# Optimization experiments

Hardware: AMD Instinct MI355X
Metric: run time of the kernel (lower is better)

Reference implementation:

```python
import jax, jax.numpy as jnp
import numpy as np

B, S, D = 4, 4096, 1024
EPS_LN = 1e-5
EPS_REC = 1e-8


def _layernorm(x, g, b):
    mu = jnp.mean(x, axis=-1, keepdims=True)
    var = jnp.mean((x - mu) ** 2, axis=-1, keepdims=True)
    return (x - mu) * jax.lax.rsqrt(var + EPS_LN) * g + b


def setup_inputs() -> dict:
    key = jax.random.key(0)
    ks = jax.random.split(key, 8)
    scale = 1.0 / np.sqrt(D)
    return {
        "x": jax.random.normal(ks[0], (B, S, D), dtype=jnp.float32),
        "x_prev": jax.random.normal(ks[1], (B, S, D), dtype=jnp.float32),
        "mu": jnp.float32(0.5),
        "decay_w": jax.random.uniform(ks[2], (D, 1), jnp.float32, -scale, scale),
        "decay_b": jnp.zeros((1,), jnp.float32),
        "ln1_g": jnp.ones((D,), jnp.float32),
        "ln1_b": jnp.zeros((D,), jnp.float32),
        "Wr_w": jax.random.uniform(ks[3], (D, D), jnp.float32, -scale, scale),
        "Wr_b": jnp.zeros((D,), jnp.float32),
        "Wv_w": jax.random.uniform(ks[4], (D, D), jnp.float32, -scale, scale),
        "Wv_b": jnp.zeros((D,), jnp.float32),
        "ln2_g": jnp.ones((D,), jnp.float32),
        "ln2_b": jnp.zeros((D,), jnp.float32),
    }


def reference(x, x_prev, mu, decay_w, decay_b, ln1_g, ln1_b,
              Wr_w, Wr_b, Wv_w, Wv_b, ln2_g, ln2_b):
    # Shift (token-mix by scalar mu)
    shifted = mu * x + (1.0 - mu) * x_prev  # [B,S,D]

    # SequenceMergingSeq with C = V = W = shifted
    decay = jax.nn.sigmoid(jnp.einsum("bsd,do->bso", shifted, decay_w) + decay_b)  # [B,S,1]
    e = jnp.exp(shifted)                       # [B,S,D]
    ea = jnp.sum(e, axis=-1, keepdims=True)    # [B,S,1]
    ev = e * shifted                           # [B,S,D]

    def step(carry, inp):
        a, b = carry
        d_t, ea_t, ev_t = inp
        a = d_t * a + ea_t            # [B,1]
        b = d_t * b + ev_t            # [B,D]
        return (a, b), b / (a + EPS_REC)

    init = (jnp.zeros((B, 1), shifted.dtype), jnp.zeros((B, D), shifted.dtype))
    xs = (jnp.swapaxes(decay, 0, 1), jnp.swapaxes(ea, 0, 1), jnp.swapaxes(ev, 0, 1))
    _, out_sbd = jax.lax.scan(step, init, xs)  # [S,B,D]
    merged = _layernorm(jnp.swapaxes(out_sbd, 0, 1), ln1_g, ln1_b)  # [B,S,D]

    # StateCoupling
    gate = jax.nn.sigmoid(jnp.einsum("bsd,ed->bse", merged, Wr_w) + Wr_b)
    value = jnp.einsum("bsd,ed->bse", merged, Wv_w) + Wv_b
    coupled = _layernorm(gate * value, ln2_g, ln2_b)

    return shifted + coupled
```

## Files before the change

kernel.cpp:

```cpp
#include <hip/hip_runtime.h>

#define BATCH 4
#define SEQ   4096
#define DIM   1024
#define NCH   512
#define CHK   8
#define NROWS (BATCH*SEQ)
#define NKT   32

typedef __attribute__((ext_vector_type(4))) float f32x4;
typedef __attribute__((ext_vector_type(8))) short shortx8;
typedef __attribute__((ext_vector_type(4))) short shortx4;

static __device__ __forceinline__ unsigned short f2bf(float f){
    unsigned int u = __float_as_uint(f);
    u += 0x7FFFu + ((u >> 16) & 1u);
    return (unsigned short)(u >> 16);
}
static __device__ __forceinline__ float bf2f(unsigned short h){
    return __uint_as_float(((unsigned int)h) << 16);
}
static __device__ __forceinline__ float sigmoidf_fast(float x){
    return 1.0f / (1.0f + __expf(-x));
}
static __device__ __forceinline__ shortx4 pack4(f32x4 s){
    shortx4 o;
    o.x = (short)f2bf(s.x); o.y = (short)f2bf(s.y);
    o.z = (short)f2bf(s.z); o.w = (short)f2bf(s.w);
    return o;
}
static __device__ __forceinline__ f32x4 unpack4(shortx4 s){
    f32x4 o;
    o.x = bf2f((unsigned short)s.x); o.y = bf2f((unsigned short)s.y);
    o.z = bf2f((unsigned short)s.z); o.w = bf2f((unsigned short)s.w);
    return o;
}

__global__ __launch_bounds__(256) void k_shift_scan(
    const float* __restrict__ X, const float* __restrict__ XP,
    const float* __restrict__ mu_p, const float* __restrict__ dw,
    const float* __restrict__ db_p,
    const float* __restrict__ Wr, const float* __restrict__ Wv,
    unsigned short* __restrict__ Wcat,
    unsigned short* __restrict__ shifted,
    unsigned short* __restrict__ b_local, float* __restrict__ a_local,
    float* __restrict__ cumP)
{
    const int tid  = threadIdx.x;

    if (blockIdx.x >= 512){
        const int pb = blockIdx.x - 512;
        #pragma unroll 4
        for (int i = 0; i < 32; ++i){
            const int n = pb*32 + i;
            const int grp = n >> 5, r = n & 31;
            const float* src = (r < 16) ? (Wr + (size_t)(grp*16 + r)*DIM)
                                        : (Wv + (size_t)(grp*16 + (r-16))*DIM);
            f32x4 v = reinterpret_cast<const f32x4*>(src)[tid];
            reinterpret_cast<shortx4*>(Wcat)[n*256 + tid] = pack4(v);
        }
        return;
    }

    const int lane = tid & 63;
    const int wid  = tid >> 6;
    const int cid  = blockIdx.x*4 + wid;
    const int batch = cid >> 9;
    const int chunk = cid & (NCH-1);
    const int row0  = batch*SEQ + chunk*CHK;

    const float mu = mu_p[0];
    const float om = 1.0f - mu;
    const float db = db_p[0];

    const f32x4* dwv = reinterpret_cast<const f32x4*>(dw);
    const f32x4 w0 = dwv[lane], w1 = dwv[64+lane], w2 = dwv[128+lane], w3 = dwv[192+lane];

    f32x4 b0 = {0,0,0,0}, b1 = {0,0,0,0}, b2 = {0,0,0,0}, b3 = {0,0,0,0};
    float a_run = 0.f, cp = 1.f;

    const f32x4* Xv  = reinterpret_cast<const f32x4*>(X);
    const f32x4* XPv = reinterpret_cast<const f32x4*>(XP);
    shortx4* BL = reinterpret_cast<shortx4*>(b_local);
    shortx4* SH = reinterpret_cast<shortx4*>(shifted);

    for (int r = 0; r < CHK; ++r){
        const int row = row0 + r;
        const int rb  = row*(DIM/4);

        f32x4 x0 = Xv[rb+lane],     x1 = Xv[rb+64+lane],
              x2 = Xv[rb+128+lane], x3 = Xv[rb+192+lane];
        f32x4 p0 = XPv[rb+lane],     p1 = XPv[rb+64+lane],
              p2 = XPv[rb+128+lane], p3 = XPv[rb+192+lane];
        f32x4 s0 = mu*x0 + om*p0, s1 = mu*x1 + om*p1;
        f32x4 s2 = mu*x2 + om*p2, s3 = mu*x3 + om*p3;

        SH[rb+lane]     = pack4(s0);
        SH[rb+64+lane]  = pack4(s1);
        SH[rb+128+lane] = pack4(s2);
        SH[rb+192+lane] = pack4(s3);

        float dot = s0.x*w0.x + s0.y*w0.y + s0.z*w0.z + s0.w*w0.w
                  + s1.x*w1.x + s1.y*w1.y + s1.z*w1.z + s1.w*w1.w
                  + s2.x*w2.x + s2.y*w2.y + s2.z*w2.z + s2.w*w2.w
                  + s3.x*w3.x + s3.y*w3.y + s3.z*w3.z + s3.w*w3.w;

        f32x4 e0, e1, e2, e3;
        e0.x=__expf(s0.x); e0.y=__expf(s0.y); e0.z=__expf(s0.z); e0.w=__expf(s0.w);
        e1.x=__expf(s1.x); e1.y=__expf(s1.y); e1.z=__expf(s1.z); e1.w=__expf(s1.w);
        e2.x=__expf(s2.x); e2.y=__expf(s2.y); e2.z=__expf(s2.z); e2.w=__expf(s2.w);
        e3.x=__expf(s3.x); e3.y=__expf(s3.y); e3.z=__expf(s3.z); e3.w=__expf(s3.w);
        float ea = e0.x+e0.y+e0.z+e0.w + e1.x+e1.y+e1.z+e1.w
                 + e2.x+e2.y+e2.z+e2.w + e3.x+e3.y+e3.z+e3.w;

        #pragma unroll
        for (int off = 1; off < 64; off <<= 1){
            dot += __shfl_xor(dot, off, 64);
            ea  += __shfl_xor(ea,  off, 64);
        }

        const float dt = sigmoidf_fast(dot + db);
        a_run = dt*a_run + ea;
        cp   *= dt;
        b0 = dt*b0 + e0*s0;  b1 = dt*b1 + e1*s1;
        b2 = dt*b2 + e2*s2;  b3 = dt*b3 + e3*s3;

        BL[rb+lane]     = pack4(b0);
        BL[rb+64+lane]  = pack4(b1);
        BL[rb+128+lane] = pack4(b2);
        BL[rb+192+lane] = pack4(b3);
        if (lane == 0){ a_local[row] = a_run; cumP[row] = cp; }
    }
}

__global__ __launch_bounds__(64) void k_combine(
    const unsigned short* __restrict__ b_local, const float* __restrict__ a_local,
    const float* __restrict__ cumP,
    float* __restrict__ carryA, unsigned short* __restrict__ carryB)
{
    const int batch = blockIdx.x >> 2;
    const int dseg  = blockIdx.x & 3;
    const int tid = threadIdx.x;
    const int d0 = dseg*256 + tid*4;

    __shared__ float sP[NCH], sA[NCH];
    for (int c = tid; c < NCH; c += 64){
        const int er = batch*SEQ + c*CHK + (CHK-1);
        sP[c] = cumP[er];
        sA[c] = a_local[er];
    }
    __syncthreads();

    const unsigned short* bl = b_local + (size_t)batch*SEQ*DIM + d0;
    unsigned short* cB = carryB + (size_t)batch*NCH*DIM + d0;
    const bool wA = (dseg == 0 && tid == 0);
    float* cAp = carryA + batch*NCH;

    shortx4 pf[16];
    #pragma unroll
    for (int i = 0; i < 16; ++i)
        pf[i] = *reinterpret_cast<const shortx4*>(bl + (i*CHK + CHK-1)*DIM);

    f32x4 cb = {0,0,0,0};
    float ca = 0.f;

    for (int cc = 0; cc < NCH; cc += 16){
        const bool more = (cc + 16 < NCH);
        #pragma unroll
        for (int k = 0; k < 16; ++k){
            const int c = cc + k;
            f32x4 v = unpack4(pf[k]);
            if (more)
                pf[k] = *reinterpret_cast<const shortx4*>(bl + ((c+16)*CHK + CHK-1)*DIM);
            *reinterpret_cast<shortx4*>(cB + (size_t)c*DIM) = pack4(cb);
            if (wA) cAp[c] = ca;
            const float p = sP[c];
            cb = p*cb + v;
            ca = p*ca + sA[c];
        }
    }
}

__global__ __launch_bounds__(256) void k_fix_ln1(
    const unsigned short* __restrict__ b_local, const float* __restrict__ a_local,
    const float* __restrict__ cumP, const float* __restrict__ carryA,
    const unsigned short* __restrict__ carryB,
    const float* __restrict__ g1, const float* __restrict__ bb1,
    unsigned short* __restrict__ merged)
{
    const int tid = threadIdx.x, lane = tid & 63, wid = tid >> 6;
    const int row = blockIdx.x*4 + wid;
    const int batch = row >> 12;
    const int c = (row & (SEQ-1)) >> 3;

    const float cpv = cumP[row];
    const float a = a_local[row] + cpv * carryA[batch*NCH + c];
    const float inv_a = 1.0f / (a + 1e-8f);

    const shortx4* BL = reinterpret_cast<const shortx4*>(b_local) + (size_t)row*256;
    const shortx4* CB = reinterpret_cast<const shortx4*>(carryB) + (size_t)(batch*NCH + c)*256;

    f32x4 o[4];
    float s = 0.f, s2 = 0.f;
    #pragma unroll
    for (int j = 0; j < 4; ++j){
        f32x4 bl = unpack4(BL[j*64 + lane]);
        f32x4 cb = unpack4(CB[j*64 + lane]);
        f32x4 v = (bl + cpv*cb) * inv_a;
        o[j] = v;
        s  += v.x+v.y+v.z+v.w;
        s2 += v.x*v.x + v.y*v.y + v.z*v.z + v.w*v.w;
    }
    #pragma unroll
    for (int off = 1; off < 64; off <<= 1){
        s  += __shfl_xor(s,  off, 64);
        s2 += __shfl_xor(s2, off, 64);
    }
    const float mean = s * (1.0f/DIM);
    const float rstd = rsqrtf(s2*(1.0f/DIM) - mean*mean + 1e-5f);
    shortx4* MG = reinterpret_cast<shortx4*>(merged) + (size_t)row*256;
    #pragma unroll
    for (int j = 0; j < 4; ++j){
        f32x4 gg = reinterpret_cast<const f32x4*>(g1)[j*64 + lane];
        f32x4 bb = reinterpret_cast<const f32x4*>(bb1)[j*64 + lane];
        MG[j*64 + lane] = pack4((o[j] - mean)*rstd*gg + bb);
    }
}

typedef __attribute__((address_space(3))) unsigned int lds_uint;
typedef __attribute__((address_space(1))) unsigned int glob_uint;
static __device__ __forceinline__ void gload16(const unsigned short* g, char* l){
    __builtin_amdgcn_global_load_lds((const glob_uint*)g, (lds_uint*)l, 16, 0, 0);
}
#define SBAR() do { __builtin_amdgcn_sched_barrier(0); __builtin_amdgcn_s_barrier(); __builtin_amdgcn_sched_barrier(0); } while(0)
#define LGKM0() do { asm volatile("s_waitcnt lgkmcnt(0)" ::: "memory"); __builtin_amdgcn_sched_barrier(0); } while(0)
#define VMC(n)  asm volatile("s_waitcnt vmcnt(" #n ")" ::: "memory")
#define LDSE 136

__global__ __launch_bounds__(512, 2) void k_gemm(
    const unsigned short* __restrict__ A,
    const unsigned short* __restrict__ Bt,
    const float* __restrict__ rbias, const float* __restrict__ vbias,
    unsigned short* __restrict__ gv)
{
    __shared__ __align__(16) char lds[69632];
    const int tid  = threadIdx.x;
    const int lane = tid & 63;
    const int wid  = tid >> 6;
    const int wm   = wid >> 2;
    const int wn   = wid & 3;

    const int bid  = blockIdx.x;
    const int wgid = (bid & 7)*64 + (bid >> 3);
    const int mt = wgid >> 3, nt = wgid & 7;
    const int m0 = mt*256, n0 = nt*256;

    const int rin = lane >> 2;
    const int scg = (lane & 3) ^ (((lane >> 5) & 1) << 1);
    const unsigned short* gA = A  + (size_t)(m0 + wid*32 + rin)*DIM + scg*8;
    const unsigned short* gB = Bt + (size_t)(n0 + wid*32 + rin)*DIM + scg*8;

    const int fr = lane & 15, fq = lane >> 4;
    const int soff = fr*64 + ((fq*16) ^ ((fr & 8) ? 32 : 0));

    f32x4 acc[8][4];
    #pragma unroll
    for (int i = 0; i < 8; ++i)
        #pragma unroll
        for (int j = 0; j < 4; ++j) acc[i][j] = (f32x4){0,0,0,0};

    auto STAGE = [&](int tk){
        char* da = lds + (tk & 1)*32768 + wid*2048;
        const unsigned short* sa = gA + tk*32;
        gload16(sa,          da);
        gload16(sa + 16*DIM, da + 1024);
        char* db = lds + (tk & 1)*32768 + 16384 + wid*2048;
        const unsigned short* sb = gB + tk*32;
        gload16(sb,          db);
        gload16(sb + 16*DIM, db + 1024);
    };

    shortx8 afA[8], bfA[4], afB[8], bfB[4];

    #define LOADF(AF, BF, bb) do {                                              \
        _Pragma("unroll")                                                       \
        for (int mf = 0; mf < 8; ++mf)                                          \
            AF[mf] = *reinterpret_cast<const shortx8*>((bb) + (wm*8 + mf)*1024 + soff); \
        _Pragma("unroll")                                                       \
        for (int nf = 0; nf < 4; ++nf)                                          \
            BF[nf] = *reinterpret_cast<const shortx8*>((bb) + 16384 + (wn*4 + nf)*1024 + soff); \
    } while (0)

    #define MFMA32(AF, BF) do {                                                 \
        __builtin_amdgcn_s_setprio(1);                                          \
        _Pragma("unroll")                                                       \
        for (int mf = 0; mf < 8; ++mf)                                          \
            _Pragma("unroll")                                                   \
            for (int nf = 0; nf < 4; ++nf)                                      \
                acc[mf][nf] = __builtin_amdgcn_mfma_f32_16x16x32_bf16(          \
                    AF[mf], BF[nf], acc[mf][nf], 0, 0, 0);                      \
        __builtin_amdgcn_s_setprio(0);                                          \
    } while (0)

    #define BODY(T, AFc, BFc, AFn, BFn) do {                                    \
        LGKM0();                                                                \
        SBAR();                          \
        if ((T) + 2 < NKT){ STAGE((T) + 2); VMC(4); }                           \
        else if ((T) + 2 == NKT){ VMC(0); }                                     \
        SBAR();                          \
        if ((T) + 1 < NKT){ LOADF(AFn, BFn, lds + (((T) + 1) & 1)*32768); }     \
        __builtin_amdgcn_sched_barrier(0);                                      \
        MFMA32(AFc, BFc);                                                       \
    } while (0)

    STAGE(0); STAGE(1);
    VMC(4);
    SBAR();
    LOADF(afA, bfA, lds);

    for (int T = 0; T < NKT; T += 2){
        BODY(T,     afA, bfA, afB, bfB);
        BODY(T + 1, afB, bfB, afA, bfA);
    }

    __syncthreads();
    unsigned short* ep = reinterpret_cast<unsigned short*>(lds);
    #pragma unroll
    for (int pr = 0; pr < 2; ++pr){
        const int el = wn*32 + pr*16 + fr;
        const float rbe = rbias[nt*128 + el];
        const float vbe = vbias[nt*128 + el];
        #pragma unroll
        for (int mf = 0; mf < 8; ++mf){
            const int rbase = wm*128 + mf*16 + fq*4;
            f32x4 ga = acc[mf][2*pr], va = acc[mf][2*pr+1];
            #pragma unroll
            for (int q = 0; q < 4; ++q){
                const float g = sigmoidf_fast(ga[q] + rbe);
                ep[(rbase + q)*LDSE + el] = f2bf(g*(va[q] + vbe));
            }
        }
    }
    __syncthreads();
    #pragma unroll
    for (int p = 0; p < 8; ++p){
        const int r  = p*32 + (tid >> 4);
        const int c8 = tid & 15;
        shortx8 val = *reinterpret_cast<const shortx8*>(&ep[r*LDSE + c8*8]);
        *reinterpret_cast<shortx8*>(&gv[(size_t)(m0 + r)*DIM + nt*128 + c8*8]) = val;
    }
    #undef BODY
    #undef MFMA32
    #undef LOADF
}

__global__ __launch_bounds__(256) void k_ln2_res(
    const unsigned short* __restrict__ gvb, const unsigned short* __restrict__ shifted,
    const float* __restrict__ g2, const float* __restrict__ b2,
    float* __restrict__ out)
{
    const int tid = threadIdx.x, lane = tid & 63, wid = tid >> 6;
    const int row = blockIdx.x*4 + wid;

    const shortx4* GV = reinterpret_cast<const shortx4*>(gvb) + (size_t)row*256;
    const shortx4* SH = reinterpret_cast<const shortx4*>(shifted) + (size_t)row*256;

    f32x4 v[4];
    float s = 0.f, s2 = 0.f;
    #pragma unroll
    for (int j = 0; j < 4; ++j){
        f32x4 x = unpack4(GV[j*64 + lane]);
        v[j] = x;
        s  += x.x+x.y+x.z+x.w;
        s2 += x.x*x.x + x.y*x.y + x.z*x.z + x.w*x.w;
    }
    #pragma unroll
    for (int off = 1; off < 64; off <<= 1){
        s  += __shfl_xor(s,  off, 64);
        s2 += __shfl_xor(s2, off, 64);
    }
    const float mean = s * (1.0f/DIM);
    const float rstd = rsqrtf(s2*(1.0f/DIM) - mean*mean + 1e-5f);
    f32x4* O = reinterpret_cast<f32x4*>(out) + (size_t)row*256;
    #pragma unroll
    for (int j = 0; j < 4; ++j){
        f32x4 gg = reinterpret_cast<const f32x4*>(g2)[j*64 + lane];
        f32x4 bb = reinterpret_cast<const f32x4*>(b2)[j*64 + lane];
        f32x4 sh = unpack4(SH[j*64 + lane]);
        O[j*64 + lane] = sh + (v[j] - mean)*rstd*gg + bb;
    }
}

extern "C" void kernel_launch(void* const* d_in, const int* in_sizes, int n_in,
                              void* d_out, int out_size, void* d_ws, size_t ws_size,
                              hipStream_t stream)
{
    (void)in_sizes; (void)n_in; (void)out_size; (void)ws_size;
    const float* x     = (const float*)d_in[0];
    const float* xprev = (const float*)d_in[1];
    const float* mu    = (const float*)d_in[2];
    const float* dw    = (const float*)d_in[3];
    const float* db    = (const float*)d_in[4];
    const float* ln1g  = (const float*)d_in[5];
    const float* ln1b  = (const float*)d_in[6];
    const float* Wr    = (const float*)d_in[7];
    const float* Wrb   = (const float*)d_in[8];
    const float* Wv    = (const float*)d_in[9];
    const float* Wvb   = (const float*)d_in[10];
    const float* ln2g  = (const float*)d_in[11];
    const float* ln2b  = (const float*)d_in[12];
    float* out = (float*)d_out;

    char* ws = (char*)d_ws;
    size_t off = 0;
    auto alloc = [&](size_t bytes) -> void* {
        void* p = ws + off;
        off += (bytes + 255) & ~(size_t)255;
        return p;
    };
    unsigned short* shifted = (unsigned short*)alloc((size_t)NROWS*DIM*2);
    unsigned short* b_local = (unsigned short*)alloc((size_t)NROWS*DIM*2);
    unsigned short* merged  = (unsigned short*)alloc((size_t)NROWS*DIM*2);
    unsigned short* carryB  = (unsigned short*)alloc((size_t)BATCH*NCH*DIM*2);
    unsigned short* Wcat    = (unsigned short*)alloc((size_t)2048*1024*2);
    float* a_local          = (float*)alloc((size_t)NROWS*4);
    float* cumP             = (float*)alloc((size_t)NROWS*4);
    float* carryA           = (float*)alloc((size_t)BATCH*NCH*4);
    unsigned short* gvbuf   = b_local;

    hipLaunchKernelGGL(k_shift_scan, dim3(576),  dim3(256), 0, stream,
                       x, xprev, mu, dw, db, Wr, Wv, Wcat, shifted, b_local, a_local, cumP);
    hipLaunchKernelGGL(k_combine,    dim3(16),   dim3(64),  0, stream,
                       b_local, a_local, cumP, carryA, carryB);
    hipLaunchKernelGGL(k_fix_ln1,    dim3(4096), dim3(256), 0, stream,
                       b_local, a_local, cumP, carryA, carryB, ln1g, ln1b, merged);
    hipLaunchKernelGGL(k_gemm,       dim3(512),  dim3(512), 0, stream,
                       merged, Wcat, Wrb, Wvb, gvbuf);
    hipLaunchKernelGGL(k_ln2_res,    dim3(4096), dim3(256), 0, stream,
                       gvbuf, shifted, ln2g, ln2b, out);
}
```

Baseline: 210.6 us.

## Restructure GEMM to 4 waves with 128x128 per-wave tiles and simpler pipeline

The fused gate/value GEMM now runs with 256 threads (4 waves) per block instead of 512. Each wave computes an 8x8 grid of MFMA fragments rather than 8x4, and the software-pipelined fragment double-buffering is replaced by a single-buffered load-then-compute loop with a global prefetch two tiles ahead. The epilogue is split into two halves so the LDS staging buffer still fits. This raises arithmetic intensity per wave and cuts LDS fragment reads, but it roughly doubles accumulator registers, halves waves per CU, and loses overlap of LDS reads with MFMA.

```diff
diff --git a/kernel.cpp b/kernel.cpp
--- a/kernel.cpp
+++ b/kernel.cpp
@@ -234,10 +234,10 @@
 }
 #define SBAR() do { __builtin_amdgcn_sched_barrier(0); __builtin_amdgcn_s_barrier(); __builtin_amdgcn_sched_barrier(0); } while(0)
 #define LGKM0() do { asm volatile("s_waitcnt lgkmcnt(0)" ::: "memory"); __builtin_amdgcn_sched_barrier(0); } while(0)
-#define VMC(n)  asm volatile("s_waitcnt vmcnt(" #n ")" ::: "memory")
+#define VMC(n)  do { asm volatile("s_waitcnt vmcnt(" #n ")" ::: "memory"); __builtin_amdgcn_sched_barrier(0); } while(0)
 #define LDSE 136
 
-__global__ __launch_bounds__(512, 2) void k_gemm(
+__global__ __launch_bounds__(256, 1) void k_gemm(
     const unsigned short* __restrict__ A,
     const unsigned short* __restrict__ Bt,
     const float* __restrict__ rbias, const float* __restrict__ vbias,
@@ -247,8 +247,8 @@
     const int tid  = threadIdx.x;
     const int lane = tid & 63;
     const int wid  = tid >> 6;
-    const int wm   = wid >> 2;
-    const int wn   = wid & 3;
+    const int wm   = wid >> 1;
+    const int wn   = wid & 1;
 
     const int bid  = blockIdx.x;
     const int wgid = (bid & 7)*64 + (bid >> 3);
@@ -257,101 +257,95 @@
 
     const int rin = lane >> 2;
     const int scg = (lane & 3) ^ (((lane >> 5) & 1) << 1);
-    const unsigned short* gA = A  + (size_t)(m0 + wid*32 + rin)*DIM + scg*8;
-    const unsigned short* gB = Bt + (size_t)(n0 + wid*32 + rin)*DIM + scg*8;
+    const unsigned short* gA = A  + (size_t)(m0 + wid*64 + rin)*DIM + scg*8;
+    const unsigned short* gB = Bt + (size_t)(n0 + wid*64 + rin)*DIM + scg*8;
 
     const int fr = lane & 15, fq = lane >> 4;
     const int soff = fr*64 + ((fq*16) ^ ((fr & 8) ? 32 : 0));
 
-    f32x4 acc[8][4];
+    f32x4 acc[8][8];
     #pragma unroll
     for (int i = 0; i < 8; ++i)
         #pragma unroll
-        for (int j = 0; j < 4; ++j) acc[i][j] = (f32x4){0,0,0,0};
+        for (int j = 0; j < 8; ++j) acc[i][j] = (f32x4){0,0,0,0};
 
     auto STAGE = [&](int tk){
-        char* da = lds + (tk & 1)*32768 + wid*2048;
+        char* base = lds + (tk & 1)*32768;
         const unsigned short* sa = gA + tk*32;
-        gload16(sa,          da);
-        gload16(sa + 16*DIM, da + 1024);
-        char* db = lds + (tk & 1)*32768 + 16384 + wid*2048;
         const unsigned short* sb = gB + tk*32;
-        gload16(sb,          db);
-        gload16(sb + 16*DIM, db + 1024);
+        #pragma unroll
+        for (int s = 0; s < 4; ++s){
+            gload16(sa + (size_t)(s*16)*DIM, base + (wid*4 + s)*1024);
+            gload16(sb + (size_t)(s*16)*DIM, base + 16384 + (wid*4 + s)*1024);
+        }
     };
 
-    shortx8 afA[8], bfA[4], afB[8], bfB[4];
-
-    #define LOADF(AF, BF, bb) do {                                              \
-        _Pragma("unroll")                                                       \
-        for (int mf = 0; mf < 8; ++mf)                                          \
-            AF[mf] = *reinterpret_cast<const shortx8*>((bb) + (wm*8 + mf)*1024 + soff); \
-        _Pragma("unroll")                                                       \
-        for (int nf = 0; nf < 4; ++nf)                                          \
-            BF[nf] = *reinterpret_cast<const shortx8*>((bb) + 16384 + (wn*4 + nf)*1024 + soff); \
-    } while (0)
-
-    #define MFMA32(AF, BF) do {                                                 \
-        __builtin_amdgcn_s_setprio(1);                                          \
-        _Pragma("unroll")                                                       \
-        for (int mf = 0; mf < 8; ++mf)                                          \
-            _Pragma("unroll")                                                   \
-            for (int nf = 0; nf < 4; ++nf)                                      \
-                acc[mf][nf] = __builtin_amdgcn_mfma_f32_16x16x32_bf16(          \
-                    AF[mf], BF[nf], acc[mf][nf], 0, 0, 0);                      \
-        __builtin_amdgcn_s_setprio(0);                                          \
-    } while (0)
-
-    #define BODY(T, AFc, BFc, AFn, BFn) do {                                    \
-        LGKM0();                                                                \
-        SBAR();                          \
-        if ((T) + 2 < NKT){ STAGE((T) + 2); VMC(4); }                           \
-        else if ((T) + 2 == NKT){ VMC(0); }                                     \
-        SBAR();                          \
-        if ((T) + 1 < NKT){ LOADF(AFn, BFn, lds + (((T) + 1) & 1)*32768); }     \
-        __builtin_amdgcn_sched_barrier(0);                                      \
-        MFMA32(AFc, BFc);                                                       \
-    } while (0)
+    shortx8 af[8], bf[8];
 
     STAGE(0); STAGE(1);
-    VMC(4);
+    VMC(8);
     SBAR();
-    LOADF(afA, bfA, lds);
-
-    for (int T = 0; T < NKT; T += 2){
-        BODY(T,     afA, bfA, afB, bfB);
-        BODY(T + 1, afB, bfB, afA, bfA);
-    }
-
-    __syncthreads();
-    unsigned short* ep = reinterpret_cast<unsigned short*>(lds);
-    #pragma unroll
-    for (int pr = 0; pr < 2; ++pr){
-        const int el = wn*32 + pr*16 + fr;
-        const float rbe = rbias[nt*128 + el];
-        const float vbe = vbias[nt*128 + el];
-        #pragma unroll
-        for (int mf = 0; mf < 8; ++mf){
-            const int rbase = wm*128 + mf*16 + fq*4;
-            f32x4 ga = acc[mf][2*pr], va = acc[mf][2*pr+1];
+
+    for (int T = 0; T < NKT; ++T){
+        const char* base = lds + (T & 1)*32768;
+
+        #pragma unroll
+        for (int m = 0; m < 8; ++m)
+            af[m] = *reinterpret_cast<const shortx8*>(base + (wm*8 + m)*1024 + soff);
+        #pragma unroll
+        for (int n = 0; n < 8; ++n)
+            bf[n] = *reinterpret_cast<const shortx8*>(base + 16384 + (wn*8 + n)*1024 + soff);
+        LGKM0();
+        SBAR();
+
+        if (T + 2 < NKT) STAGE(T + 2);
+
+        __builtin_amdgcn_s_setprio(1);
+        #pragma unroll
+        for (int m = 0; m < 8; ++m)
             #pragma unroll
-            for (int q = 0; q < 4; ++q){
-                const float g = sigmoidf_fast(ga[q] + rbe);
-                ep[(rbase + q)*LDSE + el] = f2bf(g*(va[q] + vbe));
+            for (int n = 0; n < 8; ++n)
+                acc[m][n] = __builtin_amdgcn_mfma_f32_16x16x32_bf16(af[m], bf[n], acc[m][n], 0, 0, 0);
+        __builtin_amdgcn_s_setprio(0);
+
+        if (T + 1 < NKT){
+            if (T + 2 < NKT) { VMC(8); } else { VMC(0); }
+            SBAR();
+        }
+    }
+
+    #pragma unroll
+    for (int half = 0; half < 2; ++half){
+        __syncthreads();
+        unsigned short* ep = reinterpret_cast<unsigned short*>(lds);
+        if (wm == half){
+            #pragma unroll
+            for (int j = 0; j < 4; ++j){
+                const int ecol = wn*64 + j*16 + fr;
+                const float rbe = rbias[nt*128 + ecol];
+                const float vbe = vbias[nt*128 + ecol];
+                #pragma unroll
+                for (int m = 0; m < 8; ++m){
+                    const int rbase = m*16 + fq*4;
+                    f32x4 ga = acc[m][2*j], va = acc[m][2*j+1];
+                    #pragma unroll
+                    for (int q = 0; q < 4; ++q){
+                        const float g = sigmoidf_fast(ga[q] + rbe);
+                        ep[(rbase + q)*LDSE + ecol] = f2bf(g*(va[q] + vbe));
+                    }
+                }
             }
         }
-    }
-    __syncthreads();
-    #pragma unroll
-    for (int p = 0; p < 8; ++p){
-        const int r  = p*32 + (tid >> 4);
-        const int c8 = tid & 15;
-        shortx8 val = *reinterpret_cast<const shortx8*>(&ep[r*LDSE + c8*8]);
-        *reinterpret_cast<shortx8*>(&gv[(size_t)(m0 + r)*DIM + nt*128 + c8*8]) = val;
-    }
-    #undef BODY
-    #undef MFMA32
-    #undef LOADF
+        __syncthreads();
+        #pragma unroll
+        for (int p = 0; p < 8; ++p){
+            const int r  = p*16 + (tid >> 4);
+            const int c8 = tid & 15;
+            shortx8 val = *reinterpret_cast<const shortx8*>(&ep[r*LDSE + c8*8]);
+            *reinterpret_cast<shortx8*>(
+                &gv[(size_t)(m0 + half*128 + r)*DIM + nt*128 + c8*8]) = val;
+        }
+    }
 }
 
 __global__ __launch_bounds__(256) void k_ln2_res(
@@ -434,7 +428,7 @@
                        b_local, a_local, cumP, carryA, carryB);
     hipLaunchKernelGGL(k_fix_ln1,    dim3(4096), dim3(256), 0, stream,
                        b_local, a_local, cumP, carryA, carryB, ln1g, ln1b, merged);
-    hipLaunchKernelGGL(k_gemm,       dim3(512),  dim3(512), 0, stream,
+    hipLaunchKernelGGL(k_gemm,       dim3(512),  dim3(256), 0, stream,
                        merged, Wcat, Wrb, Wvb, gvbuf);
     hipLaunchKernelGGL(k_ln2_res,    dim3(4096), dim3(256), 0, stream,
                        gvbuf, shifted, ln2g, ln2b, out);
```

Result: slower. 227.1 us (+7.8%).
